# Kernel tuning notes

Hardware: AMD Instinct MI355X
Metric: run time of the kernel (lower is better)

Reference implementation:

```python
import jax, jax.numpy as jnp
import numpy as np

DELTA = 6.0      # 3 / (1 - alpha), alpha = 0.5
ETA = 1.0
MS_ITER = 3
D_FEAT = 256
N_PTS = 8192
X_SCALE = 0.06   # keeps ||x||^2 ~ 0.9 so exp(DELTA * X^T X) is well-conditioned


def setup_inputs() -> dict:
    key = jax.random.key(0)
    X = jax.random.normal(key, (D_FEAT, N_PTS), dtype=jnp.float32) * X_SCALE
    return {"X": X}


def _mean_shift_once(X):
    # X: [d, N]
    S = jnp.einsum('dn,dm->nm', X, X)          # X^T X, [N, N]
    K = jnp.exp(DELTA * S)                     # Gaussian-like affinity, [N, N]
    colsum = jnp.sum(K, axis=0)                # d = K^T @ ones  -> column sums, [N]
    # X @ P with P = (1-eta) I + eta K D_inv; D_inv = diag(1/colsum).
    # X @ K @ D_inv == (X @ K) / colsum (per-column scaling) -- no diag/eye materialized.
    XK = X @ K                                 # [d, N]
    return (1.0 - ETA) * X + ETA * (XK / colsum[None, :])


def reference(X):
    outs = []
    cur = X
    for _ in range(MS_ITER):
        cur = _mean_shift_once(cur)
        outs.append(cur)
    return tuple(outs)
```

## Files before the change

kernel.cpp:

```cpp
#include <hip/hip_runtime.h>
#include <hip/hip_bf16.h>
#include <stdint.h>

#define DFEAT 256
#define NPTS  8192

typedef __attribute__((ext_vector_type(8)))  short bf16x8;
typedef __attribute__((ext_vector_type(16))) float f32x16;
typedef __attribute__((ext_vector_type(4)))  int   int4v;
typedef __attribute__((ext_vector_type(4)))  float f32x4;

#define AS1 __attribute__((address_space(1)))
#define AS3 __attribute__((address_space(3)))

__device__ inline void dma16(const void* g, void* l) {
  __builtin_amdgcn_global_load_lds((const AS1 uint32_t*)g, (AS3 uint32_t*)l, 16, 0, 0);
}

__device__ inline uint16_t f2bf(float f) {
  union { float f; uint32_t u; } v; v.f = f;
  return (uint16_t)((v.u + 0x7FFFu + ((v.u >> 16) & 1u)) >> 16);
}


__global__ __launch_bounds__(256, 2) void ms_fused(
    const uint16_t* __restrict__ xaf,
    const uint16_t* __restrict__ xbf,
    float* __restrict__ num,
    float* __restrict__ cs)
{
  __shared__ __attribute__((aligned(16))) uint16_t XT[2][16384];
  __shared__ __attribute__((aligned(16))) uint16_t Ps[64 * 64];

  const int tid  = threadIdx.x;
  const int w    = tid >> 6;
  const int lane = tid & 63;
  const int l31  = lane & 31;
  const int g    = lane >> 5;
  const int mt   = blockIdx.x & 127;
  const int q    = blockIdx.x >> 7;
  const int m0   = mt * 64;
  const int a_sub = w >> 1;
  const int b_sub = w & 1;

  const char* xafc = (const char*)xaf;
  const char* xbfc = (const char*)xbf;
  char*       Psc  = (char*)Ps;

  bf16x8 Bm[16];
  {
    const char* bp = xafc + (size_t)(m0 / 32 + b_sub) * 16384 + g * 512 + l31 * 16;
    #pragma unroll
    for (int ks = 0; ks < 16; ++ks)
      Bm[ks] = __builtin_bit_cast(bf16x8, *(const int4v*)(bp + ks * 1024));
  }

  f32x16 accO[2][2];
  #pragma unroll
  for (int i = 0; i < 2; ++i)
    #pragma unroll
    for (int j = 0; j < 2; ++j)
      #pragma unroll
      for (int r = 0; r < 16; ++r) accO[i][j][r] = 0.0f;
  float csacc = 0.0f;

  const int mloc = 32 * b_sub + l31;
  const int l7   = l31 & 7;
  const int j0   = q * 32;

  {
    const char* src = xafc + (size_t)j0 * 32768;
    #pragma unroll
    for (int r = 0; r < 8; ++r)
      dma16(src + tid * 16 + r * 4096, (char*)XT[0] + tid * 16 + r * 4096);
  }

  for (int t = 0; t < 32; ++t) {
    const int jt  = j0 + t;
    const int cur = t & 1;
    __syncthreads();

    if (t < 31) {
      const char* src = xafc + (size_t)(jt + 1) * 32768;
      #pragma unroll
      for (int r = 0; r < 8; ++r)
        dma16(src + tid * 16 + r * 4096,
              (char*)XT[cur ^ 1] + tid * 16 + r * 4096);
    }

    const int n0 = jt * 64;
    bf16x8 Xf[2][4];
    #pragma unroll
    for (int t2 = 0; t2 < 2; ++t2) {
      const char* xp = xbfc + (size_t)(2 * w + t2) * 524288 +
                       (size_t)(n0 >> 3) * 512 + g * 512 + l31 * 16;
      #pragma unroll
      for (int ks = 0; ks < 4; ++ks)
        Xf[t2][ks] = __builtin_bit_cast(bf16x8, *(const int4v*)(xp + ks * 1024));
    }

    f32x16 s;
    #pragma unroll
    for (int r = 0; r < 16; ++r) s[r] = 0.0f;
    {
      const char* ap = (const char*)XT[cur] + a_sub * 16384 + g * 512 + l31 * 16;
      #pragma unroll
      for (int ks = 0; ks < 16; ++ks) {
        bf16x8 A = __builtin_bit_cast(bf16x8, *(const int4v*)(ap + ks * 1024));
        s = __builtin_amdgcn_mfma_f32_32x32x16_bf16(A, Bm[ks], s, 0, 0, 0);
      }
    }

    #pragma unroll
    for (int k = 0; k < 4; ++k) {
      float e0 = __expf(6.0f * s[4*k+0]);
      float e1 = __expf(6.0f * s[4*k+1]);
      float e2 = __expf(6.0f * s[4*k+2]);
      float e3 = __expf(6.0f * s[4*k+3]);
      csacc += (e0 + e1) + (e2 + e3);
      uint32_t lo = (uint32_t)f2bf(e0) | ((uint32_t)f2bf(e1) << 16);
      uint32_t hi = (uint32_t)f2bf(e2) | ((uint32_t)f2bf(e3) << 16);
      int p = (4 * a_sub + k) ^ (mloc & 7);
      *(uint64_t*)(Psc + mloc * 128 + p * 16 + 8 * g) =
          ((uint64_t)hi << 32) | lo;
    }
    __syncthreads();

    #pragma unroll
    for (int ks = 0; ks < 4; ++ks) {
      bf16x8 Bp[2];
      #pragma unroll
      for (int mm = 0; mm < 2; ++mm) {
        int mrow = 32 * mm + l31;
        int p = (2 * ks + g) ^ l7;
        Bp[mm] = __builtin_bit_cast(bf16x8,
            *(const int4v*)(Psc + mrow * 128 + p * 16));
      }
      #pragma unroll
      for (int t2 = 0; t2 < 2; ++t2) {
        accO[t2][0] = __builtin_amdgcn_mfma_f32_32x32x16_bf16(Xf[t2][ks], Bp[0], accO[t2][0], 0,0,0);
        accO[t2][1] = __builtin_amdgcn_mfma_f32_32x32x16_bf16(Xf[t2][ks], Bp[1], accO[t2][1], 0,0,0);
      }
    }
  }

  csacc += __shfl_xor(csacc, 32, 64);
  if (g == 0) atomicAdd(&cs[m0 + mloc], csacc);
  #pragma unroll
  for (int t2 = 0; t2 < 2; ++t2)
    #pragma unroll
    for (int mm = 0; mm < 2; ++mm)
      #pragma unroll
      for (int r = 0; r < 16; ++r) {
        int drow = 32 * (2 * w + t2) + (r & 3) + 8 * (r >> 2) + 4 * g;
        int mg   = m0 + 32 * mm + l31;
        atomicAdd(&num[(size_t)drow * NPTS + mg], accO[t2][mm][r]);
      }
}

__global__ __launch_bounds__(256) void ms_combine(
    const float* __restrict__ src, const float* __restrict__ csr,
    float* __restrict__ csz, float* __restrict__ yout,
    float* __restrict__ numz,
    uint16_t* __restrict__ xaf, uint16_t* __restrict__ xbf,
    const int mode)
{
  __shared__ uint16_t T[64][66];
  const int tid = threadIdx.x;
  const int n0 = blockIdx.x * 64;
  const int d0 = blockIdx.y * 64;

  #pragma unroll
  for (int i = 0; i < 4; ++i) {
    int e  = tid + i * 256;
    int dl = e >> 4, nq = e & 15;
    size_t idx = (size_t)(d0 + dl) * NPTS + (n0 + nq * 4);
    f32x4 v = *(const f32x4*)(src + idx);
    if (mode) {
      f32x4 c = *(const f32x4*)(csr + n0 + nq * 4);
      v /= c;
      *(f32x4*)(yout + idx) = v;
      f32x4 z = {0.f, 0.f, 0.f, 0.f};
      *(f32x4*)(numz + idx) = z;
    }
    #pragma unroll
    for (int k = 0; k < 4; ++k) T[dl][nq * 4 + k] = f2bf(v[k]);
  }
  if (mode && blockIdx.y == 0 && tid < 64) csz[n0 + tid] = 0.0f;
  __syncthreads();

  char* xafc = (char*)xaf;
  char* xbfc = (char*)xbf;
  #pragma unroll
  for (int i = 0; i < 2; ++i) {
    int c  = tid + i * 256;
    int nb = c >> 8, s2 = (c >> 5) & 7, ln = c & 31;
    union { uint32_t u[4]; int4v v; } pk;
    #pragma unroll
    for (int k = 0; k < 4; ++k) {
      uint32_t lo = T[s2 * 8 + 2 * k][nb * 32 + ln];
      uint32_t hi = T[s2 * 8 + 2 * k + 1][nb * 32 + ln];
      pk.u[k] = lo | (hi << 16);
    }
    *(int4v*)(xafc + (size_t)(n0 / 32 + nb) * 16384 +
              (size_t)(d0 / 8 + s2) * 512 + ln * 16) = pk.v;
  }
  #pragma unroll
  for (int i = 0; i < 2; ++i) {
    int c  = tid + i * 256;
    int db = c >> 8, uu = (c >> 5) & 7, ln = c & 31;
    const uint16_t* tr = &T[db * 32 + ln][uu * 8];
    union { uint32_t u[4]; int4v v; } pk;
    #pragma unroll
    for (int k = 0; k < 4; ++k)
      pk.u[k] = (uint32_t)tr[2 * k] | ((uint32_t)tr[2 * k + 1] << 16);
    *(int4v*)(xbfc + (size_t)(d0 / 32 + db) * 524288 +
              (size_t)(n0 / 8 + uu) * 512 + ln * 16) = pk.v;
  }
}

extern "C" void kernel_launch(void* const* d_in, const int* in_sizes, int n_in,
                              void* d_out, int out_size, void* d_ws, size_t ws_size,
                              hipStream_t stream)
{
  (void)in_sizes; (void)n_in; (void)out_size; (void)ws_size;
  const float* X = (const float*)d_in[0];
  float* out = (float*)d_out;
  char* ws = (char*)d_ws;
  uint16_t* xaf = (uint16_t*)(ws);
  uint16_t* xbf = (uint16_t*)(ws + (4u << 20));
  float*    num = (float*)   (ws + (8u << 20));
  float*    cs0 = (float*)   (ws + (16u << 20));
  float*    cs1 = (float*)   (ws + (16u << 20) + 32768);

  hipMemsetAsync(ws + (8u << 20), 0, (8u << 20) + 65536, stream);

  dim3 cgrid(NPTS / 64, DFEAT / 64);
  ms_combine<<<cgrid, 256, 0, stream>>>(X, nullptr, nullptr, nullptr, nullptr,
                                        xaf, xbf, 0);
  for (int it = 0; it < 3; ++it) {
    float* csA = (it & 1) ? cs1 : cs0;
    float* csB = (it & 1) ? cs0 : cs1;
    ms_fused<<<512, 256, 0, stream>>>(xaf, xbf, num, csA);
    ms_combine<<<cgrid, 256, 0, stream>>>(num, csA, csB,
                                          out + (size_t)it * DFEAT * NPTS,
                                          num, xaf, xbf, 1);
  }
}
```

Before: 349.0 us.

## Remap blocks per XCD, split MFMA chains, relax mid-tile barrier, repad P tile

Several changes to the fused mean-shift kernel. Block indices are remapped so that blocks sharing a j-quarter land on the same XCD, which should improve L2 reuse. The global Xf loads are issued before the DMA prefetch. The 16-step S accumulation is split into two independent MFMA chains to hide dependency latency. The second __syncthreads becomes a barrier that waits only on LDS counters, so in-flight global DMAs are not drained. The P tile gets a 144-byte row stride and a new XOR swizzle to cut bank conflicts. The lgkm-only barrier depends on the prefetched XT buffer not being read before the next full sync, and it also assumes the Xf loads are not counted against LDS.

```diff
diff --git a/kernel.cpp b/kernel.cpp
--- a/kernel.cpp
+++ b/kernel.cpp
@@ -20,6 +20,13 @@
 __device__ inline uint16_t f2bf(float f) {
   union { float f; uint32_t u; } v; v.f = f;
   return (uint16_t)((v.u + 0x7FFFu + ((v.u >> 16) & 1u)) >> 16);
+}
+
+__device__ inline void barrier_lgkm_only() {
+  __asm__ __volatile__("" ::: "memory");
+  __builtin_amdgcn_s_waitcnt(0xC07F);
+  __builtin_amdgcn_s_barrier();
+  __asm__ __volatile__("" ::: "memory");
 }
 
 
@@ -30,15 +37,17 @@
     float* __restrict__ cs)
 {
   __shared__ __attribute__((aligned(16))) uint16_t XT[2][16384];
-  __shared__ __attribute__((aligned(16))) uint16_t Ps[64 * 64];
+  __shared__ __attribute__((aligned(16))) uint16_t Ps[64 * 72];
 
   const int tid  = threadIdx.x;
   const int w    = tid >> 6;
   const int lane = tid & 63;
   const int l31  = lane & 31;
   const int g    = lane >> 5;
-  const int mt   = blockIdx.x & 127;
-  const int q    = blockIdx.x >> 7;
+  const int bid  = blockIdx.x;
+  const int xcd  = bid & 7;
+  const int q    = xcd >> 1;
+  const int mt   = (bid >> 3) + ((xcd & 1) << 6);
   const int m0   = mt * 64;
   const int a_sub = w >> 1;
   const int b_sub = w & 1;
@@ -65,7 +74,7 @@
   float csacc = 0.0f;
 
   const int mloc = 32 * b_sub + l31;
-  const int l7   = l31 & 7;
+  const int kw   = (mloc ^ (mloc >> 3)) & 7;
   const int j0   = q * 32;
 
   {
@@ -80,6 +89,18 @@
     const int cur = t & 1;
     __syncthreads();
 
+    const int n0 = jt * 64;
+    bf16x8 Xf[2][4];
+    #pragma unroll
+    for (int t2 = 0; t2 < 2; ++t2) {
+      const char* xp = xbfc + (size_t)(2 * w + t2) * 524288 +
+                       (size_t)(n0 >> 3) * 512 + g * 512 + l31 * 16;
+      #pragma unroll
+      for (int ks = 0; ks < 4; ++ks)
+        Xf[t2][ks] = __builtin_bit_cast(bf16x8, *(const int4v*)(xp + ks * 1024));
+    }
+    __asm__ __volatile__("" ::: "memory");
+
     if (t < 31) {
       const char* src = xafc + (size_t)(jt + 1) * 32768;
       #pragma unroll
@@ -88,43 +109,34 @@
               (char*)XT[cur ^ 1] + tid * 16 + r * 4096);
     }
 
-    const int n0 = jt * 64;
-    bf16x8 Xf[2][4];
-    #pragma unroll
-    for (int t2 = 0; t2 < 2; ++t2) {
-      const char* xp = xbfc + (size_t)(2 * w + t2) * 524288 +
-                       (size_t)(n0 >> 3) * 512 + g * 512 + l31 * 16;
-      #pragma unroll
-      for (int ks = 0; ks < 4; ++ks)
-        Xf[t2][ks] = __builtin_bit_cast(bf16x8, *(const int4v*)(xp + ks * 1024));
-    }
-
-    f32x16 s;
-    #pragma unroll
-    for (int r = 0; r < 16; ++r) s[r] = 0.0f;
+    f32x16 s0, s1;
+    #pragma unroll
+    for (int r = 0; r < 16; ++r) { s0[r] = 0.0f; s1[r] = 0.0f; }
     {
       const char* ap = (const char*)XT[cur] + a_sub * 16384 + g * 512 + l31 * 16;
       #pragma unroll
-      for (int ks = 0; ks < 16; ++ks) {
-        bf16x8 A = __builtin_bit_cast(bf16x8, *(const int4v*)(ap + ks * 1024));
-        s = __builtin_amdgcn_mfma_f32_32x32x16_bf16(A, Bm[ks], s, 0, 0, 0);
+      for (int ks2 = 0; ks2 < 8; ++ks2) {
+        bf16x8 A0 = __builtin_bit_cast(bf16x8, *(const int4v*)(ap + (2*ks2) * 1024));
+        bf16x8 A1 = __builtin_bit_cast(bf16x8, *(const int4v*)(ap + (2*ks2+1) * 1024));
+        s0 = __builtin_amdgcn_mfma_f32_32x32x16_bf16(A0, Bm[2*ks2],   s0, 0, 0, 0);
+        s1 = __builtin_amdgcn_mfma_f32_32x32x16_bf16(A1, Bm[2*ks2+1], s1, 0, 0, 0);
       }
     }
 
     #pragma unroll
     for (int k = 0; k < 4; ++k) {
-      float e0 = __expf(6.0f * s[4*k+0]);
-      float e1 = __expf(6.0f * s[4*k+1]);
-      float e2 = __expf(6.0f * s[4*k+2]);
-      float e3 = __expf(6.0f * s[4*k+3]);
+      float e0 = __expf(6.0f * (s0[4*k+0] + s1[4*k+0]));
+      float e1 = __expf(6.0f * (s0[4*k+1] + s1[4*k+1]));
+      float e2 = __expf(6.0f * (s0[4*k+2] + s1[4*k+2]));
+      float e3 = __expf(6.0f * (s0[4*k+3] + s1[4*k+3]));
       csacc += (e0 + e1) + (e2 + e3);
       uint32_t lo = (uint32_t)f2bf(e0) | ((uint32_t)f2bf(e1) << 16);
       uint32_t hi = (uint32_t)f2bf(e2) | ((uint32_t)f2bf(e3) << 16);
-      int p = (4 * a_sub + k) ^ (mloc & 7);
-      *(uint64_t*)(Psc + mloc * 128 + p * 16 + 8 * g) =
+      int p = (4 * a_sub + k) ^ kw;
+      *(uint64_t*)(Psc + mloc * 144 + p * 16 + 8 * g) =
           ((uint64_t)hi << 32) | lo;
     }
-    __syncthreads();
+    barrier_lgkm_only();
 
     #pragma unroll
     for (int ks = 0; ks < 4; ++ks) {
@@ -132,9 +144,9 @@
       #pragma unroll
       for (int mm = 0; mm < 2; ++mm) {
         int mrow = 32 * mm + l31;
-        int p = (2 * ks + g) ^ l7;
+        int p = (2 * ks + g) ^ ((mrow ^ (mrow >> 3)) & 7);
         Bp[mm] = __builtin_bit_cast(bf16x8,
-            *(const int4v*)(Psc + mrow * 128 + p * 16));
+            *(const int4v*)(Psc + mrow * 144 + p * 16));
       }
       #pragma unroll
       for (int t2 = 0; t2 < 2; ++t2) {
```

New measurement: 376.6 us. +7.9%, slower.

## Load A tiles directly from global to registers, drop LDS staging and swizzle

Applied to the files above, without the earlier changes.

The fused kernel no longer double-buffers the X^T tile in shared memory through global_load_lds DMA. Each wave now loads its A fragments straight from global memory into registers, so the k-loop uses no LDS staging, and barriers wait only on LDS counters instead of all outstanding memory. The block-to-tile mapping is also remapped by XCD so that blocks sharing data land on the same chiplet's L2, and the P tile uses a padded 33-word layout with scalar 32-bit LDS accesses instead of the XOR swizzle. The trade-offs are more vector registers and global-load latency exposed before the MFMAs, and the padded layout turns each 128-bit LDS read into four 32-bit reads.

```diff
diff --git a/kernel.cpp b/kernel.cpp
--- a/kernel.cpp
+++ b/kernel.cpp
@@ -10,16 +10,16 @@
 typedef __attribute__((ext_vector_type(4)))  int   int4v;
 typedef __attribute__((ext_vector_type(4)))  float f32x4;
 
-#define AS1 __attribute__((address_space(1)))
-#define AS3 __attribute__((address_space(3)))
-
-__device__ inline void dma16(const void* g, void* l) {
-  __builtin_amdgcn_global_load_lds((const AS1 uint32_t*)g, (AS3 uint32_t*)l, 16, 0, 0);
-}
-
 __device__ inline uint16_t f2bf(float f) {
   union { float f; uint32_t u; } v; v.f = f;
   return (uint16_t)((v.u + 0x7FFFu + ((v.u >> 16) & 1u)) >> 16);
+}
+
+__device__ inline void barrier_lgkm_only() {
+  __asm__ __volatile__("" ::: "memory");
+  __builtin_amdgcn_s_waitcnt(0xC07F);
+  __builtin_amdgcn_s_barrier();
+  __asm__ __volatile__("" ::: "memory");
 }
 
 
@@ -29,23 +29,23 @@
     float* __restrict__ num,
     float* __restrict__ cs)
 {
-  __shared__ __attribute__((aligned(16))) uint16_t XT[2][16384];
-  __shared__ __attribute__((aligned(16))) uint16_t Ps[64 * 64];
+  __shared__ uint32_t Ps[64 * 33];
 
   const int tid  = threadIdx.x;
   const int w    = tid >> 6;
   const int lane = tid & 63;
   const int l31  = lane & 31;
   const int g    = lane >> 5;
-  const int mt   = blockIdx.x & 127;
-  const int q    = blockIdx.x >> 7;
+  const int bid  = blockIdx.x;
+  const int xcd  = bid & 7;
+  const int q    = xcd >> 1;
+  const int mt   = (bid >> 3) + ((xcd & 1) << 6);
   const int m0   = mt * 64;
   const int a_sub = w >> 1;
   const int b_sub = w & 1;
 
   const char* xafc = (const char*)xaf;
   const char* xbfc = (const char*)xbf;
-  char*       Psc  = (char*)Ps;
 
   bf16x8 Bm[16];
   {
@@ -65,30 +65,30 @@
   float csacc = 0.0f;
 
   const int mloc = 32 * b_sub + l31;
-  const int l7   = l31 & 7;
   const int j0   = q * 32;
 
-  {
-    const char* src = xafc + (size_t)j0 * 32768;
-    #pragma unroll
-    for (int r = 0; r < 8; ++r)
-      dma16(src + tid * 16 + r * 4096, (char*)XT[0] + tid * 16 + r * 4096);
-  }
-
   for (int t = 0; t < 32; ++t) {
-    const int jt  = j0 + t;
-    const int cur = t & 1;
-    __syncthreads();
-
-    if (t < 31) {
-      const char* src = xafc + (size_t)(jt + 1) * 32768;
-      #pragma unroll
-      for (int r = 0; r < 8; ++r)
-        dma16(src + tid * 16 + r * 4096,
-              (char*)XT[cur ^ 1] + tid * 16 + r * 4096);
-    }
-
+    const int jt = j0 + t;
     const int n0 = jt * 64;
+    barrier_lgkm_only();
+
+    bf16x8 Af[16];
+    {
+      const char* ap = xafc + (size_t)((n0 >> 5) + a_sub) * 16384 + g * 512 + l31 * 16;
+      #pragma unroll
+      for (int ks = 0; ks < 16; ++ks)
+        Af[ks] = __builtin_bit_cast(bf16x8, *(const int4v*)(ap + ks * 1024));
+    }
+
+    f32x16 s;
+    #pragma unroll
+    for (int r = 0; r < 16; ++r) s[r] = 0.0f;
+    #pragma unroll
+    for (int ks = 0; ks < 16; ++ks)
+      s = __builtin_amdgcn_mfma_f32_32x32x16_bf16(Af[ks], Bm[ks], s, 0, 0, 0);
+
+    __asm__ __volatile__("" ::: "memory");
+
     bf16x8 Xf[2][4];
     #pragma unroll
     for (int t2 = 0; t2 < 2; ++t2) {
@@ -97,18 +97,6 @@
       #pragma unroll
       for (int ks = 0; ks < 4; ++ks)
         Xf[t2][ks] = __builtin_bit_cast(bf16x8, *(const int4v*)(xp + ks * 1024));
-    }
-
-    f32x16 s;
-    #pragma unroll
-    for (int r = 0; r < 16; ++r) s[r] = 0.0f;
-    {
-      const char* ap = (const char*)XT[cur] + a_sub * 16384 + g * 512 + l31 * 16;
-      #pragma unroll
-      for (int ks = 0; ks < 16; ++ks) {
-        bf16x8 A = __builtin_bit_cast(bf16x8, *(const int4v*)(ap + ks * 1024));
-        s = __builtin_amdgcn_mfma_f32_32x32x16_bf16(A, Bm[ks], s, 0, 0, 0);
-      }
     }
 
     #pragma unroll
@@ -118,23 +106,22 @@
       float e2 = __expf(6.0f * s[4*k+2]);
       float e3 = __expf(6.0f * s[4*k+3]);
       csacc += (e0 + e1) + (e2 + e3);
-      uint32_t lo = (uint32_t)f2bf(e0) | ((uint32_t)f2bf(e1) << 16);
-      uint32_t hi = (uint32_t)f2bf(e2) | ((uint32_t)f2bf(e3) << 16);
-      int p = (4 * a_sub + k) ^ (mloc & 7);
-      *(uint64_t*)(Psc + mloc * 128 + p * 16 + 8 * g) =
-          ((uint64_t)hi << 32) | lo;
-    }
-    __syncthreads();
+      int base = mloc * 33 + 16 * a_sub + 4 * k + 2 * g;
+      Ps[base]     = (uint32_t)f2bf(e0) | ((uint32_t)f2bf(e1) << 16);
+      Ps[base + 1] = (uint32_t)f2bf(e2) | ((uint32_t)f2bf(e3) << 16);
+    }
+    barrier_lgkm_only();
 
     #pragma unroll
     for (int ks = 0; ks < 4; ++ks) {
       bf16x8 Bp[2];
       #pragma unroll
       for (int mm = 0; mm < 2; ++mm) {
-        int mrow = 32 * mm + l31;
-        int p = (2 * ks + g) ^ l7;
-        Bp[mm] = __builtin_bit_cast(bf16x8,
-            *(const int4v*)(Psc + mrow * 128 + p * 16));
+        int b = (32 * mm + l31) * 33 + (2 * ks + g) * 4;
+        union { uint32_t u[4]; bf16x8 v; } tb;
+        tb.u[0] = Ps[b];     tb.u[1] = Ps[b + 1];
+        tb.u[2] = Ps[b + 2]; tb.u[3] = Ps[b + 3];
+        Bp[mm] = tb.v;
       }
       #pragma unroll
       for (int t2 = 0; t2 < 2; ++t2) {
```

After: 376.3 us. +7.8%, slower.
